# Kernel tuning notes

Measured on AMD Instinct MI355X. Metric: run time of the kernel, lower is better.

Reference implementation:

```python
import jax, jax.numpy as jnp
import numpy as np

B, T, C, H, W = 16, 8, 2048, 16, 8
C8, C4, HW, NP = C // 8, C // 4, H * W, T // 2


def _cbr(x, w, s, b):
    # 1x1 conv + folded BN (eval-mode affine) + ReLU; x: (N, Cin, H, W), w: (Cout, Cin)
    y = jnp.einsum('oc,nchw->nohw', w, x)
    return jax.nn.relu(y * s[None, :, None, None] + b[None, :, None, None])


def setup_inputs():
    key = jax.random.key(0)
    ks = jax.random.split(key, 16)
    r = lambda i, shape, sc: jax.random.normal(ks[i], shape, jnp.float32) * sc
    return dict(
        featmap=r(0, (B, T, C, H, W), 1.0),
        re_featmap=r(1, (B * T, C, H, W), 1.0),
        vect_featmap=r(2, (B, T, C), 1.0),
        embed_feat=r(3, (B, T, 128, H, W), 1.0),
        gamma_w=r(4, (C8, C), 0.03), gamma_s=jnp.ones((C8,)), gamma_b=jnp.zeros((C8,)),
        beta_w=r(5, (C8, C), 0.03), beta_s=jnp.ones((C8,)), beta_b=jnp.zeros((C8,)),
        gg_w=r(6, (128, 2 * HW), 0.05), gg_s=jnp.ones((128,)), gg_b=jnp.zeros((128,)),
        tte_w=r(7, (128, 256), 0.05), tte_s=jnp.ones((128,)), tte_b=jnp.zeros((128,)),
        te_w=r(8, (1, 256), 0.05), te_s=jnp.ones((1,)), te_b=jnp.zeros((1,)),
        theta_w=r(9, (C8, C), 0.03), theta_b=jnp.zeros((C8,)),
        cp_w1=r(10, (C8, C4), 0.05), cp_b1=jnp.zeros((C8,)),
        cp_w2=r(11, (C, C8), 0.05), cp_b2=jnp.zeros((C,)),
    )


def reference(featmap, re_featmap, vect_featmap, embed_feat,
              gamma_w, gamma_s, gamma_b, beta_w, beta_s, beta_b,
              gg_w, gg_s, gg_b, tte_w, tte_s, tte_b, te_w, te_s, te_b,
              theta_w, theta_b, cp_w1, cp_b1, cp_w2, cp_b2):
    # spatial attention embeddings: (B, T, C8, HW)
    gamma = _cbr(re_featmap, gamma_w, gamma_s, gamma_b).reshape(B, T, C8, HW)
    beta = _cbr(re_featmap, beta_w, beta_s, beta_b).reshape(B, T, C8, HW)

    # channel attention: Conv1d over time of (B, C, T) -> (B, C8, T)
    cp = jax.nn.relu(jnp.einsum('oc,btc->bot', theta_w, vect_featmap) + theta_b[None, :, None])
    cp = cp.reshape(B, C8, NP, 2)
    c0 = cp[..., 0].transpose(0, 2, 1)  # (B, NP, C8)
    c1 = cp[..., 1].transpose(0, 2, 1)

    def mlp(x):  # (B, NP, C4) -> sigmoid gate (B, NP, C)
        h1 = jax.nn.relu(x @ cp_w1.T + cp_b1)
        return jax.nn.sigmoid(h1 @ cp_w2.T + cp_b2)

    p00 = mlp(jnp.concatenate([c0, c1], -1))  # (B, NP, C)
    p01 = mlp(jnp.concatenate([c1, c0], -1))

    # pairwise spatial graphs
    g0, g1 = gamma[:, 0::2], gamma[:, 1::2]  # (B, NP, C8, HW)
    b0, b1 = beta[:, 0::2], beta[:, 1::2]
    Gs0 = jnp.einsum('bpcs,bpct->bpst', g0, b1)  # (B, NP, HW, HW)
    Gs1 = jnp.einsum('bpcs,bpct->bpst', g1, b0)
    # Gs_in = Gs^T viewed as (HW, H, W); Gs_out = Gs viewed likewise
    j0 = jnp.concatenate([Gs0.transpose(0, 1, 3, 2), Gs1], 2).reshape(B * NP, 2 * HW, H, W)
    j1 = jnp.concatenate([Gs1.transpose(0, 1, 3, 2), Gs0], 2).reshape(B * NP, 2 * HW, H, W)
    gj0 = _cbr(j0, gg_w, gg_s, gg_b)  # (B*NP, 128, H, W)
    gj1 = _cbr(j1, gg_w, gg_s, gg_b)

    ef = embed_feat.reshape(B, NP, 2, 128, H, W)
    e0 = ef[:, :, 0].reshape(B * NP, 128, H, W)
    e1 = ef[:, :, 1].reshape(B * NP, 128, H, W)
    ta = _cbr(jnp.concatenate([e0, e1], 1), tte_w, tte_s, tte_b)  # (B*NP, 128, H, W)
    tb = _cbr(jnp.concatenate([e1, e0], 1), tte_w, tte_s, tte_b)

    def gate(t_feat, gj):  # conv 256->1 + BN + sigmoid
        y = jnp.einsum('oc,nchw->nohw', te_w, jnp.concatenate([t_feat, gj], 1))
        return jax.nn.sigmoid(y * te_s[None, :, None, None] + te_b[None, :, None, None])

    pa = gate(ta, gj0).reshape(B, NP, 1, H, W)
    pb = gate(tb, gj1).reshape(B, NP, 1, H, W)

    f = featmap.reshape(B, NP, 2, C, H, W)
    gate0 = p00[..., None, None] * pa  # (B, NP, C, H, W)
    gate1 = p01[..., None, None] * pb
    out = jax.nn.relu(gate0 * f[:, :, 0] + gate1 * f[:, :, 1])
    return out * out  # (B, T//2, C, H, W)
```

## Files before the change

### kernel.cpp

```cpp
#include <hip/hip_runtime.h>
#include <stdint.h>


typedef _Float16 f16;
typedef _Float16 f16x2 __attribute__((ext_vector_type(2)));
typedef _Float16 f16x4 __attribute__((ext_vector_type(4)));
typedef _Float16 f16x8 __attribute__((ext_vector_type(8)));
typedef float f32x4 __attribute__((ext_vector_type(4)));

typedef const void __attribute__((address_space(1)))* gptr1;
typedef void __attribute__((address_space(3)))* lptr3;

__device__ __forceinline__ void gload16(const void* g, void* l) {
  __builtin_amdgcn_global_load_lds((gptr1)g, (lptr3)l, 16, 0, 0);
}

__device__ __forceinline__ float sigmoidf_(float x) { return 1.f / (1.f + expf(-x)); }

#define WAIT_VM20 asm volatile("s_waitcnt vmcnt(20)" ::: "memory")
#define WAIT_VM0 asm volatile("s_waitcnt vmcnt(0)" ::: "memory")
#define WAIT_LGKM8 asm volatile("s_waitcnt lgkmcnt(8)" ::: "memory")
#define WAIT_LGKM0 asm volatile("s_waitcnt lgkmcnt(0)" ::: "memory")
#define SBAR __builtin_amdgcn_s_barrier()
#define SCHED0 __builtin_amdgcn_sched_barrier(0)

__global__ __launch_bounds__(256) void kPP(const float* __restrict__ gw, const float* __restrict__ gs,
                                           const float* __restrict__ bw, const float* __restrict__ bs,
                                           const float* __restrict__ gg_w, const float* __restrict__ gg_s,
                                           const float* __restrict__ tte_w, const float* __restrict__ tte_s,
                                           const float* __restrict__ thw, const float* __restrict__ w1,
                                           const float* __restrict__ w2,
                                           f16* __restrict__ Wf,
                                           float* __restrict__ ggT, float* __restrict__ tteT,
                                           float* __restrict__ thwT, float* __restrict__ w1T,
                                           float* __restrict__ w2T) {
  __shared__ __align__(16) float TL[64][65];
  int t = threadIdx.x;
  int bid = blockIdx.x;
  if (bid < 512) {
    int id = bid * 256 + t;
    int o = id >> 8, cch = id & 255;
    float s; const float* row;
    if (o < 256) { s = gs[o]; row = gw + (size_t)o * 2048; }
    else         { s = bs[o - 256]; row = bw + (size_t)(o - 256) * 2048; }
    int kb = cch >> 3, sub = cch & 7;
    int subd = sub ^ (o & 7);
    f16x8 h8;
    for (int j = 0; j < 8; ++j)
      h8[j] = (f16)(row[cch * 8 + j] * s);
    size_t ob = (size_t)o * 2048 + (size_t)kb * 64 + (size_t)subd * 8;
    *(f16x8*)(Wf + ob) = h8;
    return;
  }
  int tb = bid - 512;
  const float* src; float* dst; const float* scale = nullptr; int R, C;
  if (tb < 128)      { src = thw;   dst = thwT; R = 256;  C = 2048; }
  else if (tb < 256) { tb -= 128; src = w2;  dst = w2T;  R = 2048; C = 256; }
  else if (tb < 288) { tb -= 256; src = w1;  dst = w1T;  R = 256;  C = 512; }
  else if (tb < 296) { tb -= 288; src = gg_w;  dst = ggT;  scale = gg_s;  R = 128; C = 256; }
  else               { tb -= 296; src = tte_w; dst = tteT; scale = tte_s; R = 128; C = 256; }
  int tpc = C >> 6;
  int r0 = (tb / tpc) * 64, c0 = (tb % tpc) * 64;
  int i16 = t >> 4, j4 = (t & 15) * 4;
  for (int s = 0; s < 4; ++s) {
    int i = i16 + s * 16;
    float4 v = *(const float4*)(src + (size_t)(r0 + i) * C + c0 + j4);
    TL[i][j4 + 0] = v.x; TL[i][j4 + 1] = v.y; TL[i][j4 + 2] = v.z; TL[i][j4 + 3] = v.w;
  }
  __syncthreads();
  for (int s = 0; s < 4; ++s) {
    int j = i16 + s * 16;
    float4 w;
    w.x = TL[j4 + 0][j]; w.y = TL[j4 + 1][j]; w.z = TL[j4 + 2][j]; w.w = TL[j4 + 3][j];
    if (scale) {
      w.x *= scale[r0 + j4 + 0]; w.y *= scale[r0 + j4 + 1];
      w.z *= scale[r0 + j4 + 2]; w.w *= scale[r0 + j4 + 3];
    }
    *(float4*)(dst + (size_t)(c0 + j) * R + r0 + j4) = w;
  }
}

__global__ __launch_bounds__(512, 2) void kGemm8(const float* __restrict__ X, const f16* __restrict__ Wf,
                                                 const float* __restrict__ gamma_b, const float* __restrict__ beta_b,
                                                 f16* __restrict__ gammaFh, f16* __restrict__ betaFh) {
  __shared__ __align__(16) f16 S[3][24576];
  int t = threadIdx.x;
  int lane = t & 63, wid = t >> 6;
  int wr = wid >> 2, wc = wid & 3;
  int bid = blockIdx.x;
  int bx = (bid & 7) * 16 + (bid >> 4);
  int by = (bid >> 3) & 1;
  size_t N0 = (size_t)by * 256;
  int row8 = wid * 8 + (lane >> 3);
  int sl = lane & 7;
  int fr = lane & 15, fq = lane >> 4;
  f32x4 acc[4][4] = {};
  f16x8 a[8], b[8];
  float ar0[16], ar1[16];

  const float* Xb = X + (size_t)bx * 262144;
  int hwl = lane + (wid & 1) * 64;
  int kg = wid >> 1;
  int kg16 = kg * 16;
  int woA[2];
#pragma unroll
  for (int r = 0; r < 2; ++r) {
    int cg = kg * 2 + r;
    woA[r] = hwl * 64 + ((cg ^ (hwl & 7)) << 3);
  }

  const char* WB = (const char*)Wf;
  const size_t woff0 = (N0 + row8) * 4096 + (size_t)sl * 16;
  const size_t woff1 = (N0 + 64 + row8) * 4096 + (size_t)sl * 16;
  const size_t woff2 = (N0 + 128 + row8) * 4096 + (size_t)sl * 16;
  const size_t woff3 = (N0 + 192 + row8) * 4096 + (size_t)sl * 16;

#define AISSUE(bank, s) do {                                                       \
    const float* p_ = Xb + ((s) * 64 + kg16) * 128 + hwl;                          \
    _Pragma("unroll") for (int j_ = 0; j_ < 16; ++j_)                              \
      bank[j_] = p_[j_ * 128];                                                     \
  } while (0)

#define WSTAGE(dst, s) do {                                                        \
    int koff_ = (s) << 7;                                                          \
    char* l_ = (char*)(dst) + 16384 + wid * 1024;                                  \
    gload16(WB + woff0 + koff_, l_);                                               \
    gload16(WB + woff1 + koff_, l_ + 8192);                                        \
    gload16(WB + woff2 + koff_, l_ + 16384);                                       \
    gload16(WB + woff3 + koff_, l_ + 24576);                                       \
  } while (0)

#define AWRITE(bank, dst) do {                                                     \
    f16* ad_ = (f16*)(dst);                                                        \
    _Pragma("unroll") for (int r_ = 0; r_ < 2; ++r_) {                             \
      f16x8 h_;                                                                    \
      _Pragma("unroll") for (int i_ = 0; i_ < 8; ++i_)                             \
        h_[i_] = (f16)bank[r_ * 8 + i_];                                           \
      *(f16x8*)(ad_ + woA[r_]) = h_;                                               \
    }                                                                              \
  } while (0)

#define LOADG(buf, g) do {                                                         \
    const f16* bA_ = (const f16*)(buf);                                            \
    const f16* bB_ = bA_ + 8192;                                                   \
    int cg_ = (g) * 4 + fq;                                                        \
    _Pragma("unroll") for (int mi = 0; mi < 4; ++mi) {                             \
      int m_ = wr * 64 + mi * 16 + fr;                                             \
      a[(g) * 4 + mi] = *(const f16x8*)(bA_ + m_ * 64 + ((cg_ ^ (m_ & 7)) << 3));  \
    }                                                                              \
    _Pragma("unroll") for (int ni = 0; ni < 4; ++ni) {                             \
      int n_ = wc * 64 + ni * 16 + fr;                                             \
      b[(g) * 4 + ni] = *(const f16x8*)(bB_ + n_ * 64 + ((cg_ ^ (n_ & 7)) << 3));  \
    }                                                                              \
  } while (0)

#define MFMA_G(g) do {                                                             \
    _Pragma("unroll") for (int mi = 0; mi < 4; ++mi)                               \
      _Pragma("unroll") for (int ni = 0; ni < 4; ++ni)                             \
        acc[mi][ni] = __builtin_amdgcn_mfma_f32_16x16x32_f16(                      \
            a[(g) * 4 + mi], b[(g) * 4 + ni], acc[mi][ni], 0, 0, 0);               \
  } while (0)

#define STEP(cur, nxt, n2, s, BI, BW) do {                                         \
    SBAR;                                                                          \
    if ((s) <= 29) { AISSUE(BI, (s) + 2); WSTAGE(n2, (s) + 2); }                   \
    SCHED0;                                                                        \
    LOADG(cur, 0);                                                                 \
    SCHED0;                                                                        \
    LOADG(cur, 1);                                                                 \
    WAIT_LGKM8;                                                                    \
    SCHED0;                                                                        \
    __builtin_amdgcn_s_setprio(1);                                                 \
    MFMA_G(0);                                                                     \
    if ((s) <= 30) {                                                               \
      if ((s) <= 29) { WAIT_VM20; } else { WAIT_VM0; }                             \
      SCHED0;                                                                      \
      AWRITE(BW, nxt);                                                             \
      WAIT_LGKM8;                                                                  \
      SCHED0;                                                                      \
      MFMA_G(1);                                                                   \
      __builtin_amdgcn_s_setprio(0);                                               \
      WAIT_LGKM0;                                                                  \
    } else {                                                                       \
      WAIT_LGKM0;                                                                  \
      SCHED0;                                                                      \
      MFMA_G(1);                                                                   \
      __builtin_amdgcn_s_setprio(0);                                               \
    }                                                                              \
  } while (0)

  AISSUE(ar0, 0); WSTAGE(&S[0][0], 0);
  SCHED0;
  AISSUE(ar1, 1); WSTAGE(&S[1][0], 1);
  SCHED0;
  WAIT_VM20;
  SCHED0;
  AWRITE(ar0, &S[0][0]);
  WAIT_LGKM0;

  for (int base = 0; base < 30; base += 6) {
    STEP(&S[0][0], &S[1][0], &S[2][0], base + 0, ar0, ar1);
    STEP(&S[1][0], &S[2][0], &S[0][0], base + 1, ar1, ar0);
    STEP(&S[2][0], &S[0][0], &S[1][0], base + 2, ar0, ar1);
    STEP(&S[0][0], &S[1][0], &S[2][0], base + 3, ar1, ar0);
    STEP(&S[1][0], &S[2][0], &S[0][0], base + 4, ar0, ar1);
    STEP(&S[2][0], &S[0][0], &S[1][0], base + 5, ar1, ar0);
  }
  STEP(&S[0][0], &S[1][0], &S[2][0], 30, ar0, ar1);
  STEP(&S[1][0], &S[2][0], &S[0][0], 31, ar1, ar0);
#undef STEP
#undef MFMA_G
#undef LOADG
#undef AWRITE
#undef WSTAGE
#undef AISSUE

  const float* bias = by ? beta_b : gamma_b;
  f16* outb = by ? betaFh : gammaFh;
#pragma unroll
  for (int mi = 0; mi < 4; ++mi) {
    int hwb = wr * 64 + mi * 16 + fq * 4;
#pragma unroll
    for (int ni = 0; ni < 4; ++ni) {
      int o = wc * 64 + ni * 16 + fr;
      float bb = bias[o];
      f32x4 v = acc[mi][ni];
      f16x4 w;
      w[0] = (f16)fmaxf(v[0] + bb, 0.f);
      w[1] = (f16)fmaxf(v[1] + bb, 0.f);
      w[2] = (f16)fmaxf(v[2] + bb, 0.f);
      w[3] = (f16)fmaxf(v[3] + bb, 0.f);
      *(f16x4*)(outb + (size_t)bx * 32768 + (size_t)o * 128 + hwb) = w;
    }
  }
}

__global__ __launch_bounds__(256) void kTT(const float* __restrict__ vect, const float* __restrict__ thwT,
                                           float* __restrict__ P,
                                           const float* __restrict__ embed, const float* __restrict__ tteT,
                                           const float* __restrict__ tte_b, const float* __restrict__ te_w,
                                           float* __restrict__ Sta) {
  __shared__ float V[512];
  __shared__ __align__(16) float E[256 * 64];
  __shared__ float Red[16 * 64];
  int bid = blockIdx.x;
  int t = threadIdx.x;
  if (bid < 512) {
    int bt = bid & 127, kq = bid >> 7;
    const float* src = vect + (size_t)bt * 2048 + kq * 512;
    if (t < 128) *(float4*)(V + t * 4) = *(const float4*)(src + t * 4);
    __syncthreads();
    const float* wp = thwT + (size_t)kq * 512 * 256 + t;
    float acc = 0.f;
#pragma unroll 8
    for (int c = 0; c < 512; ++c)
      acc = fmaf(wp[(size_t)c * 256], V[c], acc);
    P[((size_t)kq * 128 + bt) * 256 + t] = acc;
    return;
  }
  int i = bid - 512;
  int n = i & 63, gate = (i >> 6) & 1, hh = (i >> 7) & 1;
  int b = n >> 2, p = n & 3;
  const float* eA = embed + (size_t)(b * 8 + 2 * p + gate) * 16384 + hh * 64;
  const float* eB = embed + (size_t)(b * 8 + 2 * p + 1 - gate) * 16384 + hh * 64;
  for (int r = 0; r < 8; ++r) {
    int f = r * 256 + t;
    int ch = f >> 4, q = (f & 15) * 4;
    *(float4*)(E + ch * 64 + q) = *(const float4*)(eA + (size_t)ch * 128 + q);
  }
  for (int r = 0; r < 8; ++r) {
    int f = r * 256 + t;
    int ch = f >> 4, q = (f & 15) * 4;
    *(float4*)(E + (128 + ch) * 64 + q) = *(const float4*)(eB + (size_t)ch * 128 + q);
  }
  __syncthreads();
  int ty = t >> 4, tx = t & 15;
  float acc[8][4] = {};
  for (int c = 0; c < 256; ++c) {
    float w8[8];
    *(float4*)w8 = *(const float4*)(tteT + (size_t)c * 128 + ty * 8);
    *(float4*)(w8 + 4) = *(const float4*)(tteT + (size_t)c * 128 + ty * 8 + 4);
    float4 g = *(const float4*)(E + c * 64 + tx * 4);
    for (int ii = 0; ii < 8; ++ii) {
      acc[ii][0] = fmaf(w8[ii], g.x, acc[ii][0]);
      acc[ii][1] = fmaf(w8[ii], g.y, acc[ii][1]);
      acc[ii][2] = fmaf(w8[ii], g.z, acc[ii][2]);
      acc[ii][3] = fmaf(w8[ii], g.w, acc[ii][3]);
    }
  }
  float par[4] = {0.f, 0.f, 0.f, 0.f};
  for (int ii = 0; ii < 8; ++ii) {
    int o = ty * 8 + ii;
    float tb = tte_b[o], tw = te_w[o];
    for (int j = 0; j < 4; ++j)
      par[j] += tw * fmaxf(acc[ii][j] + tb, 0.f);
  }
  for (int j = 0; j < 4; ++j) Red[ty * 64 + tx * 4 + j] = par[j];
  __syncthreads();
  if (t < 64) {
    float s = 0.f;
    for (int g = 0; g < 16; ++g) s += Red[g * 64 + t];
    Sta[(size_t)gate * 8192 + n * 128 + hh * 64 + t] = s;
  }
}

__global__ __launch_bounds__(256) void kAG(const float* __restrict__ P, const float* __restrict__ thb,
                                           const float* __restrict__ w1T, const float* __restrict__ b1,
                                           float* __restrict__ h1,
                                           const f16* __restrict__ gammaFh, const f16* __restrict__ betaFh,
                                           float* __restrict__ Gs0, float* __restrict__ Gs1) {
  __shared__ float x0[256], x1[256];
  __shared__ float ra[256], rb[256];
  __shared__ __align__(16) float As[16 * 128];
  __shared__ __align__(16) float Bs[16 * 64];
  int bid = blockIdx.x;
  int t = threadIdx.x;
  if (bid < 256) {
    int bp = bid & 63, och = bid >> 6;
    int b = bp >> 2, p = bp & 3;
    int bt0 = b * 8 + 2 * p, bt1 = bt0 + 1;
    {
      float a0 = 0.f, a1 = 0.f;
      for (int q = 0; q < 4; ++q) {
        a0 += P[((size_t)q * 128 + bt0) * 256 + t];
        a1 += P[((size_t)q * 128 + bt1) * 256 + t];
      }
      float tb = thb[t];
      x0[t] = fmaxf(a0 + tb, 0.f);
      x1[t] = fmaxf(a1 + tb, 0.f);
    }
    __syncthreads();
    int o = och * 64 + (t & 63);
    int ks = t >> 6;
    const float* xa = (ks < 2) ? x0 : x1;
    const float* xb = (ks < 2) ? x1 : x0;
    int kbase = ks * 128;
    int xoff = (ks < 2) ? kbase : kbase - 256;
    float aa = 0.f, ab = 0.f;
#pragma unroll 8
    for (int ii = 0; ii < 128; ++ii) {
      float w = w1T[(size_t)(kbase + ii) * 256 + o];
      aa = fmaf(w, xa[xoff + ii], aa);
      ab = fmaf(w, xb[xoff + ii], ab);
    }
    ra[t] = aa;
    rb[t] = ab;
    __syncthreads();
    if (t < 64) {
      float sa = ra[t] + ra[64 + t] + ra[128 + t] + ra[192 + t];
      float sb = rb[t] + rb[64 + t] + rb[128 + t] + rb[192 + t];
      float bb = b1[o];
      h1[((size_t)bp * 2) * 256 + o] = fmaxf(sa + bb, 0.f);
      h1[((size_t)bp * 2 + 1) * 256 + o] = fmaxf(sb + bb, 0.f);
    }
    return;
  }
  int i = bid - 256;
  int n = i & 63, which = (i >> 6) & 1, th = (i >> 7) & 1;
  int b = n >> 2, p = n & 3;
  int tg = 2 * p + which;
  int tb = 2 * p + 1 - which;
  const f16* A = gammaFh + (size_t)(b * 8 + tg) * 32768;
  const f16* Bm = betaFh + (size_t)(b * 8 + tb) * 32768;
  float* out = (which ? Gs1 : Gs0) + (size_t)n * 16384;
  int ty = t >> 4, tx = t & 15;
  float acc[8][4] = {};
  for (int c0 = 0; c0 < 256; c0 += 16) {
    {
      int cc = t >> 4, col8 = (t & 15) * 8;
      f16x8 v = *(const f16x8*)(A + (size_t)(c0 + cc) * 128 + col8);
      for (int j = 0; j < 8; ++j) As[cc * 128 + col8 + j] = (float)v[j];
    }
    if (t < 128) {
      int cc = t >> 3, col8 = (t & 7) * 8;
      f16x8 v = *(const f16x8*)(Bm + (size_t)(c0 + cc) * 128 + th * 64 + col8);
      for (int j = 0; j < 8; ++j) Bs[cc * 64 + col8 + j] = (float)v[j];
    }
    __syncthreads();
    for (int cc = 0; cc < 16; ++cc) {
      float a8[8];
      *(float4*)a8 = *(const float4*)(As + cc * 128 + ty * 8);
      *(float4*)(a8 + 4) = *(const float4*)(As + cc * 128 + ty * 8 + 4);
      float4 b4 = *(const float4*)(Bs + cc * 64 + tx * 4);
      for (int ii = 0; ii < 8; ++ii) {
        acc[ii][0] = fmaf(a8[ii], b4.x, acc[ii][0]);
        acc[ii][1] = fmaf(a8[ii], b4.y, acc[ii][1]);
        acc[ii][2] = fmaf(a8[ii], b4.z, acc[ii][2]);
        acc[ii][3] = fmaf(a8[ii], b4.w, acc[ii][3]);
      }
    }
    __syncthreads();
  }
  for (int ii = 0; ii < 8; ++ii) {
    *(float4*)(out + (size_t)(ty * 8 + ii) * 128 + th * 64 + tx * 4) =
        make_float4(acc[ii][0], acc[ii][1], acc[ii][2], acc[ii][3]);
  }
}

__global__ __launch_bounds__(256) void kBG(const float* __restrict__ h1, const float* __restrict__ w2T,
                                           const float* __restrict__ b2,
                                           float* __restrict__ p00, float* __restrict__ p01,
                                           const float* __restrict__ Gs0, const float* __restrict__ Gs1,
                                           const float* __restrict__ ggT, const float* __restrict__ gg_b,
                                           const float* __restrict__ te_w, float* __restrict__ Sgj) {
  __shared__ float ha[256], hb[256];
  __shared__ float G0h[64 * 129];
  __shared__ __align__(16) float G1c[128 * 64];
  __shared__ float Red[16 * 64];
  int bid = blockIdx.x;
  int t = threadIdx.x;
  if (bid < 512) {
    int bp = bid & 63, chc = bid >> 6;
    ha[t] = h1[((size_t)bp * 2) * 256 + t];
    hb[t] = h1[((size_t)bp * 2 + 1) * 256 + t];
    __syncthreads();
    int ch = chc * 256 + t;
    float sa = 0.f, sb = 0.f;
#pragma unroll 8
    for (int k = 0; k < 256; ++k) {
      float w = w2T[(size_t)k * 2048 + ch];
      sa = fmaf(w, ha[k], sa);
      sb = fmaf(w, hb[k], sb);
    }
    p00[(size_t)bp * 2048 + ch] = sigmoidf_(sa + b2[ch]);
    p01[(size_t)bp * 2048 + ch] = sigmoidf_(sb + b2[ch]);
    return;
  }
  int i = bid - 512;
  int n = i & 63, gate = (i >> 6) & 1, hh = (i >> 7) & 1;
  const float* srcT = (gate == 0 ? Gs0 : Gs1) + (size_t)n * 16384;
  const float* srcC = (gate == 0 ? Gs1 : Gs0) + (size_t)n * 16384;
  for (int r = 0; r < 8; ++r) {
    int f = r * 256 + t;
    int hwl = f >> 5, c4 = (f & 31) * 4;
    float4 v = *(const float4*)(srcT + (size_t)(hh * 64 + hwl) * 128 + c4);
    G0h[hwl * 129 + c4 + 0] = v.x;
    G0h[hwl * 129 + c4 + 1] = v.y;
    G0h[hwl * 129 + c4 + 2] = v.z;
    G0h[hwl * 129 + c4 + 3] = v.w;
  }
  for (int r = 0; r < 8; ++r) {
    int f = r * 256 + t;
    int c = f >> 4, q = (f & 15) * 4;
    *(float4*)(G1c + c * 64 + q) = *(const float4*)(srcC + (size_t)c * 128 + hh * 64 + q);
  }
  __syncthreads();
  int ty = t >> 4, tx = t & 15;
  float acc[8][4] = {};
  for (int c = 0; c < 128; ++c) {
    float w8[8];
    *(float4*)w8 = *(const float4*)(ggT + (size_t)c * 128 + ty * 8);
    *(float4*)(w8 + 4) = *(const float4*)(ggT + (size_t)c * 128 + ty * 8 + 4);
    float g4[4];
    for (int j = 0; j < 4; ++j) g4[j] = G0h[(tx * 4 + j) * 129 + c];
    for (int ii = 0; ii < 8; ++ii)
      for (int j = 0; j < 4; ++j)
        acc[ii][j] = fmaf(w8[ii], g4[j], acc[ii][j]);
  }
  for (int c = 0; c < 128; ++c) {
    float w8[8];
    *(float4*)w8 = *(const float4*)(ggT + (size_t)(128 + c) * 128 + ty * 8);
    *(float4*)(w8 + 4) = *(const float4*)(ggT + (size_t)(128 + c) * 128 + ty * 8 + 4);
    float4 g = *(const float4*)(G1c + c * 64 + tx * 4);
    for (int ii = 0; ii < 8; ++ii) {
      acc[ii][0] = fmaf(w8[ii], g.x, acc[ii][0]);
      acc[ii][1] = fmaf(w8[ii], g.y, acc[ii][1]);
      acc[ii][2] = fmaf(w8[ii], g.z, acc[ii][2]);
      acc[ii][3] = fmaf(w8[ii], g.w, acc[ii][3]);
    }
  }
  float par[4] = {0.f, 0.f, 0.f, 0.f};
  for (int ii = 0; ii < 8; ++ii) {
    int o = ty * 8 + ii;
    float gb = gg_b[o], tw = te_w[128 + o];
    for (int j = 0; j < 4; ++j)
      par[j] += tw * fmaxf(acc[ii][j] + gb, 0.f);
  }
  for (int j = 0; j < 4; ++j) Red[ty * 64 + tx * 4 + j] = par[j];
  __syncthreads();
  if (t < 64) {
    float s = 0.f;
    for (int g = 0; g < 16; ++g) s += Red[g * 64 + t];
    Sgj[(size_t)gate * 8192 + n * 128 + hh * 64 + t] = s;
  }
}

__global__ __launch_bounds__(256) void kFinal(const float* __restrict__ featmap, const float* __restrict__ p00,
                                              const float* __restrict__ p01, const float* __restrict__ Sta,
                                              const float* __restrict__ Sgj, const float* __restrict__ te_s,
                                              const float* __restrict__ te_b, float* __restrict__ out) {
  int fid = blockIdx.x * 256 + threadIdx.x;
  int h4 = (fid & 31) * 4;
  int c = (fid >> 5) & 2047;
  int bp = fid >> 16;
  int b = bp >> 2, p = bp & 3;
  float ga = p00[(size_t)bp * 2048 + c];
  float gb = p01[(size_t)bp * 2048 + c];
  float ts = te_s[0], tbv = te_b[0];
  float4 sa0 = *(const float4*)(Sta + (size_t)bp * 128 + h4);
  float4 sg0 = *(const float4*)(Sgj + (size_t)bp * 128 + h4);
  float4 sa1 = *(const float4*)(Sta + 8192 + (size_t)bp * 128 + h4);
  float4 sg1 = *(const float4*)(Sgj + 8192 + (size_t)bp * 128 + h4);
  float4 pa4, pb4;
  pa4.x = sigmoidf_(ts * (sa0.x + sg0.x) + tbv);
  pa4.y = sigmoidf_(ts * (sa0.y + sg0.y) + tbv);
  pa4.z = sigmoidf_(ts * (sa0.z + sg0.z) + tbv);
  pa4.w = sigmoidf_(ts * (sa0.w + sg0.w) + tbv);
  pb4.x = sigmoidf_(ts * (sa1.x + sg1.x) + tbv);
  pb4.y = sigmoidf_(ts * (sa1.y + sg1.y) + tbv);
  pb4.z = sigmoidf_(ts * (sa1.z + sg1.z) + tbv);
  pb4.w = sigmoidf_(ts * (sa1.w + sg1.w) + tbv);
  const float* f0 = featmap + (size_t)(b * 8 + 2 * p) * 262144 + (size_t)c * 128 + h4;
  const float* f1 = f0 + 262144;
  float4 v0 = *(const float4*)f0;
  float4 v1 = *(const float4*)f1;
  float4 o4;
  float r;
  r = fmaxf(ga * pa4.x * v0.x + gb * pb4.x * v1.x, 0.f); o4.x = r * r;
  r = fmaxf(ga * pa4.y * v0.y + gb * pb4.y * v1.y, 0.f); o4.y = r * r;
  r = fmaxf(ga * pa4.z * v0.z + gb * pb4.z * v1.z, 0.f); o4.z = r * r;
  r = fmaxf(ga * pa4.w * v0.w + gb * pb4.w * v1.w, 0.f); o4.w = r * r;
  *(float4*)(out + (size_t)fid * 4) = o4;
}

extern "C" void kernel_launch(void* const* d_in, const int* in_sizes, int n_in,
                              void* d_out, int out_size, void* d_ws, size_t ws_size,
                              hipStream_t stream) {
  (void)in_sizes; (void)n_in; (void)out_size; (void)ws_size;
  const float* featmap    = (const float*)d_in[0];
  const float* re_featmap = (const float*)d_in[1];
  const float* vect       = (const float*)d_in[2];
  const float* embed      = (const float*)d_in[3];
  const float* gamma_w    = (const float*)d_in[4];
  const float* gamma_s    = (const float*)d_in[5];
  const float* gamma_b    = (const float*)d_in[6];
  const float* beta_w     = (const float*)d_in[7];
  const float* beta_s     = (const float*)d_in[8];
  const float* beta_b     = (const float*)d_in[9];
  const float* gg_w       = (const float*)d_in[10];
  const float* gg_s       = (const float*)d_in[11];
  const float* gg_b       = (const float*)d_in[12];
  const float* tte_w      = (const float*)d_in[13];
  const float* tte_s      = (const float*)d_in[14];
  const float* tte_b      = (const float*)d_in[15];
  const float* te_w       = (const float*)d_in[16];
  const float* te_s       = (const float*)d_in[17];
  const float* te_b       = (const float*)d_in[18];
  const float* theta_w    = (const float*)d_in[19];
  const float* theta_b    = (const float*)d_in[20];
  const float* cp_w1      = (const float*)d_in[21];
  const float* cp_b1      = (const float*)d_in[22];
  const float* cp_w2      = (const float*)d_in[23];
  const float* cp_b2      = (const float*)d_in[24];
  float* out = (float*)d_out;

  char* w = (char*)d_ws;
  f16* Wf  = (f16*)w;   w += (size_t)512 * 2048 * 2;
  f16* gammaFh = (f16*)w; w += (size_t)128 * 256 * 128 * 2;
  f16* betaFh  = (f16*)w; w += (size_t)128 * 256 * 128 * 2;
  float* Gs0    = (float*)w; w += (size_t)64 * 128 * 128 * 4;
  float* Gs1    = (float*)w; w += (size_t)64 * 128 * 128 * 4;
  float* ggT    = (float*)w; w += (size_t)256 * 128 * 4;
  float* tteT   = (float*)w; w += (size_t)256 * 128 * 4;
  float* thwT   = (float*)w; w += (size_t)2048 * 256 * 4;
  float* w1T    = (float*)w; w += (size_t)512 * 256 * 4;
  float* w2T    = (float*)w; w += (size_t)256 * 2048 * 4;
  float* P      = (float*)w; w += (size_t)4 * 128 * 256 * 4;
  float* h1     = (float*)w; w += (size_t)64 * 2 * 256 * 4;
  float* Sta    = (float*)w; w += (size_t)2 * 64 * 128 * 4;
  float* Sgj    = (float*)w; w += (size_t)2 * 64 * 128 * 4;
  float* p00    = (float*)w; w += (size_t)64 * 2048 * 4;
  float* p01    = (float*)w; w += (size_t)64 * 2048 * 4;

  kPP<<<816, 256, 0, stream>>>(gamma_w, gamma_s, beta_w, beta_s, gg_w, gg_s, tte_w, tte_s,
                               theta_w, cp_w1, cp_w2, Wf, ggT, tteT, thwT, w1T, w2T);
  kGemm8<<<256, 512, 0, stream>>>(re_featmap, Wf, gamma_b, beta_b, gammaFh, betaFh);
  kTT<<<768, 256, 0, stream>>>(vect, thwT, P, embed, tteT, tte_b, te_w, Sta);
  kAG<<<512, 256, 0, stream>>>(P, theta_b, w1T, cp_b1, h1, gammaFh, betaFh, Gs0, Gs1);
  kBG<<<768, 256, 0, stream>>>(h1, w2T, cp_b2, p00, p01, Gs0, Gs1, ggT, gg_b, te_w, Sgj);
  kFinal<<<16384, 256, 0, stream>>>(featmap, p00, p01, Sta, Sgj, te_s, te_b, out);
}
```

Baseline: 234.1 us.

## Halve GEMM M-tile, double grid, switch to double-buffered pipeline

The gamma/beta projection GEMM now gives each block 64 spatial positions instead of 128. This doubles the grid to 512 blocks and shrinks LDS from a triple buffer to a double buffer, so more blocks can be resident (launch bounds raised to 4). The intent is better occupancy and fuller CU coverage. In exchange, the prefetch depth drops from two stages to one, a full vmcnt(0) wait is added each step, and each block loads the weight tile with half the reuse.

```diff
diff --git a/kernel.cpp b/kernel.cpp
--- a/kernel.cpp
+++ b/kernel.cpp
@@ -17,9 +17,10 @@
 
 __device__ __forceinline__ float sigmoidf_(float x) { return 1.f / (1.f + expf(-x)); }
 
-#define WAIT_VM20 asm volatile("s_waitcnt vmcnt(20)" ::: "memory")
+#define WAIT_VM4 asm volatile("s_waitcnt vmcnt(4)" ::: "memory")
 #define WAIT_VM0 asm volatile("s_waitcnt vmcnt(0)" ::: "memory")
-#define WAIT_LGKM8 asm volatile("s_waitcnt lgkmcnt(8)" ::: "memory")
+#define WAIT_LGKM6 asm volatile("s_waitcnt lgkmcnt(6)" ::: "memory")
+#define WAIT_LGKM1 asm volatile("s_waitcnt lgkmcnt(1)" ::: "memory")
 #define WAIT_LGKM0 asm volatile("s_waitcnt lgkmcnt(0)" ::: "memory")
 #define SBAR __builtin_amdgcn_s_barrier()
 #define SCHED0 __builtin_amdgcn_sched_barrier(0)
@@ -80,34 +81,29 @@
   }
 }
 
-__global__ __launch_bounds__(512, 2) void kGemm8(const float* __restrict__ X, const f16* __restrict__ Wf,
+__global__ __launch_bounds__(512, 4) void kGemm8(const float* __restrict__ X, const f16* __restrict__ Wf,
                                                  const float* __restrict__ gamma_b, const float* __restrict__ beta_b,
                                                  f16* __restrict__ gammaFh, f16* __restrict__ betaFh) {
-  __shared__ __align__(16) f16 S[3][24576];
+  __shared__ __align__(16) f16 S[2][20480];
   int t = threadIdx.x;
   int lane = t & 63, wid = t >> 6;
   int wr = wid >> 2, wc = wid & 3;
   int bid = blockIdx.x;
-  int bx = (bid & 7) * 16 + (bid >> 4);
+  int bx = (bid & 7) * 32 + (bid >> 4);
   int by = (bid >> 3) & 1;
+  int n = bx >> 1, hh = bx & 1;
   size_t N0 = (size_t)by * 256;
   int row8 = wid * 8 + (lane >> 3);
   int sl = lane & 7;
   int fr = lane & 15, fq = lane >> 4;
-  f32x4 acc[4][4] = {};
-  f16x8 a[8], b[8];
-  float ar0[16], ar1[16];
-
-  const float* Xb = X + (size_t)bx * 262144;
-  int hwl = lane + (wid & 1) * 64;
-  int kg = wid >> 1;
-  int kg16 = kg * 16;
-  int woA[2];
-#pragma unroll
-  for (int r = 0; r < 2; ++r) {
-    int cg = kg * 2 + r;
-    woA[r] = hwl * 64 + ((cg ^ (hwl & 7)) << 3);
-  }
+  f32x4 acc[2][4] = {};
+  f16x8 a[4], b[8];
+  float ar[8];
+
+  const float* Xb = X + (size_t)n * 262144 + hh * 64;
+  int hwl = lane;
+  int kg8 = wid * 8;
+  int woA = hwl * 64 + ((wid ^ (hwl & 7)) << 3);
 
   const char* WB = (const char*)Wf;
   const size_t woff0 = (N0 + row8) * 4096 + (size_t)sl * 16;
@@ -115,38 +111,35 @@
   const size_t woff2 = (N0 + 128 + row8) * 4096 + (size_t)sl * 16;
   const size_t woff3 = (N0 + 192 + row8) * 4096 + (size_t)sl * 16;
 
-#define AISSUE(bank, s) do {                                                       \
-    const float* p_ = Xb + ((s) * 64 + kg16) * 128 + hwl;                          \
-    _Pragma("unroll") for (int j_ = 0; j_ < 16; ++j_)                              \
-      bank[j_] = p_[j_ * 128];                                                     \
+#define AISSUE(s) do {                                                             \
+    const float* p_ = Xb + ((s) * 64 + kg8) * 128 + hwl;                           \
+    _Pragma("unroll") for (int j_ = 0; j_ < 8; ++j_)                               \
+      ar[j_] = p_[j_ * 128];                                                       \
   } while (0)
 
 #define WSTAGE(dst, s) do {                                                        \
     int koff_ = (s) << 7;                                                          \
-    char* l_ = (char*)(dst) + 16384 + wid * 1024;                                  \
+    char* l_ = (char*)(dst) + 8192 + wid * 1024;                                   \
     gload16(WB + woff0 + koff_, l_);                                               \
     gload16(WB + woff1 + koff_, l_ + 8192);                                        \
     gload16(WB + woff2 + koff_, l_ + 16384);                                       \
     gload16(WB + woff3 + koff_, l_ + 24576);                                       \
   } while (0)
 
-#define AWRITE(bank, dst) do {                                                     \
-    f16* ad_ = (f16*)(dst);                                                        \
-    _Pragma("unroll") for (int r_ = 0; r_ < 2; ++r_) {                             \
-      f16x8 h_;                                                                    \
-      _Pragma("unroll") for (int i_ = 0; i_ < 8; ++i_)                             \
-        h_[i_] = (f16)bank[r_ * 8 + i_];                                           \
-      *(f16x8*)(ad_ + woA[r_]) = h_;                                               \
-    }                                                                              \
+#define AWRITE(dst) do {                                                           \
+    f16x8 h_;                                                                      \
+    _Pragma("unroll") for (int i_ = 0; i_ < 8; ++i_)                               \
+      h_[i_] = (f16)ar[i_];                                                        \
+    *(f16x8*)((f16*)(dst) + woA) = h_;                                             \
   } while (0)
 
 #define LOADG(buf, g) do {                                                         \
     const f16* bA_ = (const f16*)(buf);                                            \
-    const f16* bB_ = bA_ + 8192;                                                   \
+    const f16* bB_ = bA_ + 4096;                                                   \
     int cg_ = (g) * 4 + fq;                                                        \
-    _Pragma("unroll") for (int mi = 0; mi < 4; ++mi) {                             \
-      int m_ = wr * 64 + mi * 16 + fr;                                             \
-      a[(g) * 4 + mi] = *(const f16x8*)(bA_ + m_ * 64 + ((cg_ ^ (m_ & 7)) << 3));  \
+    _Pragma("unroll") for (int mi = 0; mi < 2; ++mi) {                             \
+      int m_ = wr * 32 + mi * 16 + fr;                                             \
+      a[(g) * 2 + mi] = *(const f16x8*)(bA_ + m_ * 64 + ((cg_ ^ (m_ & 7)) << 3));  \
     }                                                                              \
     _Pragma("unroll") for (int ni = 0; ni < 4; ++ni) {                             \
       int n_ = wc * 64 + ni * 16 + fr;                                             \
@@ -155,32 +148,33 @@
   } while (0)
 
 #define MFMA_G(g) do {                                                             \
-    _Pragma("unroll") for (int mi = 0; mi < 4; ++mi)                               \
+    _Pragma("unroll") for (int mi = 0; mi < 2; ++mi)                               \
       _Pragma("unroll") for (int ni = 0; ni < 4; ++ni)                             \
         acc[mi][ni] = __builtin_amdgcn_mfma_f32_16x16x32_f16(                      \
-            a[(g) * 4 + mi], b[(g) * 4 + ni], acc[mi][ni], 0, 0, 0);               \
+            a[(g) * 2 + mi], b[(g) * 4 + ni], acc[mi][ni], 0, 0, 0);               \
   } while (0)
 
-#define STEP(cur, nxt, n2, s, BI, BW) do {                                         \
+#define STEP(cur, nxt, s) do {                                                     \
     SBAR;                                                                          \
-    if ((s) <= 29) { AISSUE(BI, (s) + 2); WSTAGE(n2, (s) + 2); }                   \
+    if ((s) <= 30) { AISSUE((s) + 1); WSTAGE(nxt, (s) + 1); }                      \
     SCHED0;                                                                        \
     LOADG(cur, 0);                                                                 \
     SCHED0;                                                                        \
     LOADG(cur, 1);                                                                 \
-    WAIT_LGKM8;                                                                    \
+    WAIT_LGKM6;                                                                    \
     SCHED0;                                                                        \
     __builtin_amdgcn_s_setprio(1);                                                 \
     MFMA_G(0);                                                                     \
     if ((s) <= 30) {                                                               \
-      if ((s) <= 29) { WAIT_VM20; } else { WAIT_VM0; }                             \
+      WAIT_VM4;                                                                    \
       SCHED0;                                                                      \
-      AWRITE(BW, nxt);                                                             \
-      WAIT_LGKM8;                                                                  \
+      AWRITE(nxt);                                                                 \
+      WAIT_LGKM1;                                                                  \
       SCHED0;                                                                      \
       MFMA_G(1);                                                                   \
       __builtin_amdgcn_s_setprio(0);                                               \
       WAIT_LGKM0;                                                                  \
+      WAIT_VM0;                                                                    \
     } else {                                                                       \
       WAIT_LGKM0;                                                                  \
       SCHED0;                                                                      \
@@ -189,25 +183,18 @@
     }                                                                              \
   } while (0)
 
-  AISSUE(ar0, 0); WSTAGE(&S[0][0], 0);
+  AISSUE(0); WSTAGE(&S[0][0], 0);
   SCHED0;
-  AISSUE(ar1, 1); WSTAGE(&S[1][0], 1);
+  WAIT_VM4;
   SCHED0;
-  WAIT_VM20;
-  SCHED0;
-  AWRITE(ar0, &S[0][0]);
+  AWRITE(&S[0][0]);
+  WAIT_VM0;
   WAIT_LGKM0;
 
-  for (int base = 0; base < 30; base += 6) {
-    STEP(&S[0][0], &S[1][0], &S[2][0], base + 0, ar0, ar1);
-    STEP(&S[1][0], &S[2][0], &S[0][0], base + 1, ar1, ar0);
-    STEP(&S[2][0], &S[0][0], &S[1][0], base + 2, ar0, ar1);
-    STEP(&S[0][0], &S[1][0], &S[2][0], base + 3, ar1, ar0);
-    STEP(&S[1][0], &S[2][0], &S[0][0], base + 4, ar0, ar1);
-    STEP(&S[2][0], &S[0][0], &S[1][0], base + 5, ar1, ar0);
-  }
-  STEP(&S[0][0], &S[1][0], &S[2][0], 30, ar0, ar1);
-  STEP(&S[1][0], &S[2][0], &S[0][0], 31, ar1, ar0);
+  for (int base = 0; base < 32; base += 2) {
+    STEP(&S[0][0], &S[1][0], base);
+    STEP(&S[1][0], &S[0][0], base + 1);
+  }
 #undef STEP
 #undef MFMA_G
 #undef LOADG
@@ -218,8 +205,8 @@
   const float* bias = by ? beta_b : gamma_b;
   f16* outb = by ? betaFh : gammaFh;
 #pragma unroll
-  for (int mi = 0; mi < 4; ++mi) {
-    int hwb = wr * 64 + mi * 16 + fq * 4;
+  for (int mi = 0; mi < 2; ++mi) {
+    int hwb = wr * 32 + mi * 16 + fq * 4;
 #pragma unroll
     for (int ni = 0; ni < 4; ++ni) {
       int o = wc * 64 + ni * 16 + fr;
@@ -230,7 +217,7 @@
       w[1] = (f16)fmaxf(v[1] + bb, 0.f);
       w[2] = (f16)fmaxf(v[2] + bb, 0.f);
       w[3] = (f16)fmaxf(v[3] + bb, 0.f);
-      *(f16x4*)(outb + (size_t)bx * 32768 + (size_t)o * 128 + hwb) = w;
+      *(f16x4*)(outb + (size_t)n * 32768 + (size_t)o * 128 + hh * 64 + hwb) = w;
     }
   }
 }
@@ -574,7 +561,7 @@
 
   kPP<<<816, 256, 0, stream>>>(gamma_w, gamma_s, beta_w, beta_s, gg_w, gg_s, tte_w, tte_s,
                                theta_w, cp_w1, cp_w2, Wf, ggT, tteT, thwT, w1T, w2T);
-  kGemm8<<<256, 512, 0, stream>>>(re_featmap, Wf, gamma_b, beta_b, gammaFh, betaFh);
+  kGemm8<<<512, 512, 0, stream>>>(re_featmap, Wf, gamma_b, beta_b, gammaFh, betaFh);
   kTT<<<768, 256, 0, stream>>>(vect, thwT, P, embed, tteT, tte_b, te_w, Sta);
   kAG<<<512, 256, 0, stream>>>(P, theta_b, w1T, cp_b1, h1, gammaFh, betaFh, Gs0, Gs1);
   kBG<<<768, 256, 0, stream>>>(h1, w2T, cp_b2, p00, p01, Gs0, Gs1, ggT, gg_b, te_w, Sgj);
```

Measured after the change: 242.3 us. 3.5% more time.
